# Kernel tuning notes

Measured on AMD Instinct MI355X. Metric: run time of the kernel, lower is better.

The kernel has to match this reference:

```python
import jax, jax.numpy as jnp
import numpy as np
import math

B, S, E, H, F, L, V = 4, 256, 512, 8, 2048, 4, 32000
HD = E // H
MAXLEN = 5000  # EnhancedPositionalEncoding max_len default


def _ln(x, s, b):
    m = jnp.mean(x, axis=-1, keepdims=True)
    v = jnp.mean((x - m) ** 2, axis=-1, keepdims=True)
    return (x - m) / jnp.sqrt(v + 1e-5) * s + b


def setup_inputs() -> dict:
    key = jax.random.key(0)
    ks = jax.random.split(key, 10)
    n = lambda k, shape: jax.random.normal(k, shape, jnp.float32) * 0.02
    return {
        "src": jax.random.randint(ks[0], (B, S), 0, V),
        "emb": jax.random.uniform(ks[1], (V, E), jnp.float32, -0.1, 0.1),
        "rel_table": n(ks[2], (2 * MAXLEN - 1, E)),
        "norm_in_s": jnp.ones(E, jnp.float32), "norm_in_b": jnp.zeros(E, jnp.float32),
        "inW": n(ks[3], (L, 3 * E, E)), "inB": jnp.zeros((L, 3 * E), jnp.float32),
        "outW": n(ks[4], (L, E, E)), "outB": jnp.zeros((L, E), jnp.float32),
        "ln1_s": jnp.ones((L, E), jnp.float32), "ln1_b": jnp.zeros((L, E), jnp.float32),
        "ln2_s": jnp.ones((L, E), jnp.float32), "ln2_b": jnp.zeros((L, E), jnp.float32),
        "w1": n(ks[5], (L, F, E)), "b1": jnp.zeros((L, F), jnp.float32),
        "w2": n(ks[6], (L, E, F)), "b2": jnp.zeros((L, E), jnp.float32),
        "normf_s": jnp.ones(E, jnp.float32), "normf_b": jnp.zeros(E, jnp.float32),
        "dec_w": jax.random.uniform(ks[7], (V, E), jnp.float32, -0.1, 0.1),
        "dec_b": jnp.zeros(V, jnp.float32),
    }


def reference(src, emb, rel_table, norm_in_s, norm_in_b, inW, inB, outW, outB,
              ln1_s, ln1_b, ln2_s, ln2_b, w1, b1, w2, b2, normf_s, normf_b,
              dec_w, dec_b):
    x = emb[src] * math.sqrt(E)                 # [B,S,E], pos_encoder is identity in relative mode
    x = _ln(x, norm_in_s, norm_in_b)
    # relative-position embedding gather: idx[l,m] = (m - l) + S - 1
    pos = jnp.arange(S)
    rel_idx = (pos[None, :] - pos[:, None]) + S - 1
    rel = rel_table[rel_idx].reshape(S, S, H, HD)  # [S,S,H,hd]
    # NOTE: torch adds the BOOL triu mask to float scores -> +1.0 at masked positions
    mask = jnp.triu(jnp.ones((S, S), jnp.float32), 1)
    scale = 1.0 / math.sqrt(HD)
    for l in range(L):
        h = _ln(x, ln1_s[l], ln1_b[l])
        qkv = h @ inW[l].T + inB[l]
        q, k, v = jnp.split(qkv, 3, axis=-1)
        q = q.reshape(B, S, H, HD).transpose(0, 2, 1, 3)  # [B,H,S,hd]
        k = k.reshape(B, S, H, HD).transpose(0, 2, 1, 3)
        v = v.reshape(B, S, H, HD).transpose(0, 2, 1, 3)
        scores = jnp.einsum('bhqd,bhkd->bhqk', q, k) * scale
        bias = jnp.einsum('bhld,lmhd->bhlm', q, rel)      # relative-position bias (unscaled, as in torch)
        attn = jax.nn.softmax(scores + bias + mask, axis=-1)
        o = jnp.einsum('bhqk,bhkd->bhqd', attn, v).transpose(0, 2, 1, 3).reshape(B, S, E)
        x = x + (o @ outW[l].T + outB[l])
        h2 = _ln(x, ln2_s[l], ln2_b[l])
        ff = jax.nn.gelu(h2 @ w1[l].T + b1[l], approximate=False) @ w2[l].T + b2[l]
        x = x + ff
    x = _ln(x, normf_s, normf_b)  # encoder final norm
    return x @ dec_w.T + dec_b    # [B,S,V]
```

## Files before the change

kernel.cpp:

```cpp
#include <hip/hip_runtime.h>
#include <hip/hip_bf16.h>
#include <math.h>

#define BB 4
#define SS 256
#define EE 512
#define HH 8
#define HD 64
#define FFD 2048
#define LL 4
#define VV 32000
#define BS (BB*SS)
#define SQRT_E 22.627416997969522f
#define ATTN_SCALE 0.125f

typedef __bf16 bf16;
typedef __attribute__((ext_vector_type(4))) __bf16 bf16x4;
typedef __attribute__((ext_vector_type(8))) __bf16 bf16x8;
typedef __attribute__((ext_vector_type(4))) float f32x4;

#define GLOBAL_AS __attribute__((address_space(1)))
#define LDS_AS    __attribute__((address_space(3)))

__device__ __forceinline__ void load_lds16(const bf16* g, bf16* l) {
    __builtin_amdgcn_global_load_lds((const GLOBAL_AS unsigned int*)g,
                                     (LDS_AS unsigned int*)l, 16, 0, 0);
}

__global__ void cvt_bf16(const float* __restrict__ in, bf16* __restrict__ out, int n) {
    int i = (blockIdx.x * 256 + threadIdx.x) * 4;
    if (i < n) {
        float4 v = *(const float4*)(in + i);
        bf16x4 o;
        o[0] = (bf16)v.x; o[1] = (bf16)v.y; o[2] = (bf16)v.z; o[3] = (bf16)v.w;
        *(bf16x4*)(out + i) = o;
    }
}

template <typename OT>
__global__ void ln_kernel(const float* __restrict__ in, const float* __restrict__ sc,
                          const float* __restrict__ bi, OT* __restrict__ out) {
    int row = blockIdx.x;
    int t = threadIdx.x;
    const float* r = in + (size_t)row * EE;
    float v0 = r[t], v1 = r[t + 256];
    float sum = v0 + v1, sq = v0 * v0 + v1 * v1;
    #pragma unroll
    for (int off = 32; off; off >>= 1) {
        sum += __shfl_xor(sum, off);
        sq  += __shfl_xor(sq, off);
    }
    __shared__ float ssum[4], ssq[4];
    int wid = t >> 6, lane = t & 63;
    if (lane == 0) { ssum[wid] = sum; ssq[wid] = sq; }
    __syncthreads();
    sum = ssum[0] + ssum[1] + ssum[2] + ssum[3];
    sq  = ssq[0] + ssq[1] + ssq[2] + ssq[3];
    float mean = sum * (1.0f / EE);
    float var  = sq * (1.0f / EE) - mean * mean;
    float rstd = rsqrtf(var + 1e-5f);
    out[(size_t)row * EE + t]       = (OT)((v0 - mean) * rstd * sc[t] + bi[t]);
    out[(size_t)row * EE + t + 256] = (OT)((v1 - mean) * rstd * sc[t + 256] + bi[t + 256]);
}

__global__ void embed_ln_kernel(const int* __restrict__ src, const float* __restrict__ emb,
                                const float* __restrict__ sc, const float* __restrict__ bi,
                                float* __restrict__ out) {
    int row = blockIdx.x;
    int t = threadIdx.x;
    const float* r = emb + (size_t)src[row] * EE;
    float v0 = r[t] * SQRT_E, v1 = r[t + 256] * SQRT_E;
    float sum = v0 + v1, sq = v0 * v0 + v1 * v1;
    #pragma unroll
    for (int off = 32; off; off >>= 1) {
        sum += __shfl_xor(sum, off);
        sq  += __shfl_xor(sq, off);
    }
    __shared__ float ssum[4], ssq[4];
    int wid = t >> 6, lane = t & 63;
    if (lane == 0) { ssum[wid] = sum; ssq[wid] = sq; }
    __syncthreads();
    sum = ssum[0] + ssum[1] + ssum[2] + ssum[3];
    sq  = ssq[0] + ssq[1] + ssq[2] + ssq[3];
    float mean = sum * (1.0f / EE);
    float var  = sq * (1.0f / EE) - mean * mean;
    float rstd = rsqrtf(var + 1e-5f);
    out[(size_t)row * EE + t]       = (v0 - mean) * rstd * sc[t] + bi[t];
    out[(size_t)row * EE + t + 256] = (v1 - mean) * rstd * sc[t + 256] + bi[t + 256];
}

template <int BM, int BN, int MODE, int OBF16>
__global__ __launch_bounds__(256) void gemm_bf16(
        const bf16* __restrict__ A, const bf16* __restrict__ W,
        const float* __restrict__ bias, void* __restrict__ Cout,
        const float* __restrict__ res, int M, int N, int K) {
    constexpr int FM = BM / 32, FN = BN / 32;
    __shared__ bf16 Atile[BM * 32];
    __shared__ bf16 Btile[BN * 32];
    int tid = threadIdx.x;
    int wid = tid >> 6, lane = tid & 63;
    int wm = (wid >> 1) * (BM / 2), wn = (wid & 1) * (BN / 2);
    int bm = blockIdx.x * BM, bn = blockIdx.y * BN;

    f32x4 acc[FM][FN];
    #pragma unroll
    for (int i = 0; i < FM; i++)
        #pragma unroll
        for (int j = 0; j < FN; j++)
            acc[i][j] = (f32x4){0.f, 0.f, 0.f, 0.f};

    int mrow = lane & 15, kq = (lane >> 4) * 8;

    for (int k0 = 0; k0 < K; k0 += 32) {
        #pragma unroll
        for (int it = 0; it < BM / 64; it++) {
            int c = it * 256 + tid;
            int row = c >> 2, kc = (c & 3) * 8;
            load_lds16(A + (size_t)(bm + row) * K + k0 + kc, Atile + c * 8);
        }
        #pragma unroll
        for (int it = 0; it < BN / 64; it++) {
            int c = it * 256 + tid;
            int row = c >> 2, kc = (c & 3) * 8;
            load_lds16(W + (size_t)(bn + row) * K + k0 + kc, Btile + c * 8);
        }
        __syncthreads();

        bf16x8 af[FM], bfv[FN];
        #pragma unroll
        for (int i = 0; i < FM; i++)
            af[i] = *(const bf16x8*)(Atile + (wm + i * 16 + mrow) * 32 + kq);
        #pragma unroll
        for (int j = 0; j < FN; j++)
            bfv[j] = *(const bf16x8*)(Btile + (wn + j * 16 + mrow) * 32 + kq);
        #pragma unroll
        for (int i = 0; i < FM; i++)
            #pragma unroll
            for (int j = 0; j < FN; j++)
                acc[i][j] = __builtin_amdgcn_mfma_f32_16x16x32_bf16(af[i], bfv[j], acc[i][j], 0, 0, 0);
        __syncthreads();
    }

    #pragma unroll
    for (int i = 0; i < FM; i++) {
        int row0 = bm + wm + i * 16 + (lane >> 4) * 4;
        #pragma unroll
        for (int j = 0; j < FN; j++) {
            int col = bn + wn + j * 16 + (lane & 15);
            float bv = bias[col];
            #pragma unroll
            for (int r = 0; r < 4; r++) {
                int row = row0 + r;
                float v = acc[i][j][r] + bv;
                if (MODE == 1) v = 0.5f * v * (1.0f + erff(v * 0.7071067811865476f));
                if (MODE == 2) v += res[(size_t)row * N + col];
                if (OBF16) ((bf16*)Cout)[(size_t)row * N + col] = (bf16)v;
                else       ((float*)Cout)[(size_t)row * N + col] = v;
            }
        }
    }
}

__global__ __launch_bounds__(256) void transpose_v(const bf16* __restrict__ qkv,
                                                   bf16* __restrict__ vT) {
    int bh = blockIdx.x, kc = blockIdx.y;
    int b = bh >> 3, h = bh & 7;
    __shared__ __align__(16) bf16 tile[64 * 72];
    int t = threadIdx.x;
    #pragma unroll
    for (int it = 0; it < 2; it++) {
        int c = it * 256 + t; int r = c >> 3, ch = c & 7;
        bf16x8 v = *(const bf16x8*)(qkv + (size_t)(b * 256 + kc * 64 + r) * 1536 + 1024 + h * 64 + ch * 8);
        *(bf16x8*)(tile + r * 72 + ch * 8) = v;
    }
    __syncthreads();
    #pragma unroll
    for (int it = 0; it < 2; it++) {
        int c = it * 256 + t; int n = c >> 3, kch = c & 7;
        bf16x8 o;
        #pragma unroll
        for (int j = 0; j < 8; j++) o[j] = tile[(kch * 8 + j) * 72 + n];
        *(bf16x8*)(vT + ((size_t)(bh * 64 + n)) * 256 + kc * 64 + kch * 8) = o;
    }
}

__global__ __launch_bounds__(256) void attn_mfma(const bf16* __restrict__ qkv,
        const bf16* __restrict__ relb, const bf16* __restrict__ vT,
        bf16* __restrict__ o) {
    int blk = blockIdx.x;
    int qt = blk & 3, bh = blk >> 2;
    int h = bh & 7, b = bh >> 3;
    int q0 = qt * 64, j0 = 192 - q0;
    int tid = threadIdx.x;
    int wid = tid >> 6, lane = tid & 63;
    int l15 = lane & 15, quad = lane >> 4;
    int mr0 = wid * 16;

    __shared__ __align__(16) bf16 Qs[64 * 72];
    __shared__ __align__(16) bf16 Stg[64 * 72];
    __shared__ __align__(16) bf16 BP[64 * 264];

    const size_t qbase = (size_t)(b * 256 + q0) * 1536 + h * 64;
    #pragma unroll
    for (int it = 0; it < 2; it++) {
        int c = it * 256 + tid; int r = c >> 3, ch = c & 7;
        bf16x8 v = *(const bf16x8*)(qkv + qbase + (size_t)r * 1536 + ch * 8);
        *(bf16x8*)(Qs + r * 72 + ch * 8) = v;
    }
    __syncthreads();
    bf16x8 af0 = *(const bf16x8*)(Qs + (mr0 + l15) * 72 + quad * 8);
    bf16x8 af1 = *(const bf16x8*)(Qs + (mr0 + l15) * 72 + 32 + quad * 8);

    for (int jc = 0; jc < 5; jc++) {
        __syncthreads();
        const size_t rbase = (size_t)(j0 + jc * 64) * 512 + h * 64;
        #pragma unroll
        for (int it = 0; it < 2; it++) {
            int c = it * 256 + tid; int r = c >> 3, ch = c & 7;
            bf16x8 v = *(const bf16x8*)(relb + rbase + (size_t)r * 512 + ch * 8);
            *(bf16x8*)(Stg + r * 72 + ch * 8) = v;
        }
        __syncthreads();
        #pragma unroll
        for (int jt = 0; jt < 4; jt++) {
            f32x4 acc = (f32x4){0.f, 0.f, 0.f, 0.f};
            bf16x8 bv0 = *(const bf16x8*)(Stg + (jt * 16 + l15) * 72 + quad * 8);
            bf16x8 bv1 = *(const bf16x8*)(Stg + (jt * 16 + l15) * 72 + 32 + quad * 8);
            acc = __builtin_amdgcn_mfma_f32_16x16x32_bf16(af0, bv0, acc, 0, 0, 0);
            acc = __builtin_amdgcn_mfma_f32_16x16x32_bf16(af1, bv1, acc, 0, 0, 0);
            int jp = jc * 64 + jt * 16 + l15;
            #pragma unroll
            for (int r = 0; r < 4; r++) {
                int ll = mr0 + quad * 4 + r;
                int m = jp + ll - 63;
                if (m >= 0 && m < 256) BP[ll * 256 + m] = (bf16)acc[r];
            }
        }
    }

    f32x4 S[16];
    #pragma unroll
    for (int i = 0; i < 16; i++) S[i] = (f32x4){0.f, 0.f, 0.f, 0.f};
    for (int kc = 0; kc < 4; kc++) {
        __syncthreads();
        const size_t kbase = (size_t)(b * 256 + kc * 64) * 1536 + 512 + h * 64;
        #pragma unroll
        for (int it = 0; it < 2; it++) {
            int c = it * 256 + tid; int r = c >> 3, ch = c & 7;
            bf16x8 v = *(const bf16x8*)(qkv + kbase + (size_t)r * 1536 + ch * 8);
            *(bf16x8*)(Stg + r * 72 + ch * 8) = v;
        }
        __syncthreads();
        #pragma unroll
        for (int nt = 0; nt < 4; nt++) {
            bf16x8 bv0 = *(const bf16x8*)(Stg + (nt * 16 + l15) * 72 + quad * 8);
            bf16x8 bv1 = *(const bf16x8*)(Stg + (nt * 16 + l15) * 72 + 32 + quad * 8);
            S[kc * 4 + nt] = __builtin_amdgcn_mfma_f32_16x16x32_bf16(af0, bv0, S[kc * 4 + nt], 0, 0, 0);
            S[kc * 4 + nt] = __builtin_amdgcn_mfma_f32_16x16x32_bf16(af1, bv1, S[kc * 4 + nt], 0, 0, 0);
        }
    }

    float rmax[4] = {-1e30f, -1e30f, -1e30f, -1e30f};
    #pragma unroll
    for (int T = 0; T < 16; T++) {
        int m = T * 16 + l15;
        #pragma unroll
        for (int r = 0; r < 4; r++) {
            int ll = mr0 + quad * 4 + r;
            float v = S[T][r] * ATTN_SCALE + (float)BP[ll * 256 + m]
                      + ((m > q0 + ll) ? 1.0f : 0.0f);
            S[T][r] = v;
            rmax[r] = fmaxf(rmax[r], v);
        }
    }
    #pragma unroll
    for (int r = 0; r < 4; r++)
        #pragma unroll
        for (int d = 1; d < 16; d <<= 1)
            rmax[r] = fmaxf(rmax[r], __shfl_xor(rmax[r], d));
    float rsum[4] = {0.f, 0.f, 0.f, 0.f};
    #pragma unroll
    for (int T = 0; T < 16; T++)
        #pragma unroll
        for (int r = 0; r < 4; r++) {
            float p = expf(S[T][r] - rmax[r]);
            S[T][r] = p;
            rsum[r] += p;
        }
    #pragma unroll
    for (int r = 0; r < 4; r++)
        #pragma unroll
        for (int d = 1; d < 16; d <<= 1)
            rsum[r] += __shfl_xor(rsum[r], d);

    __syncthreads();
    #pragma unroll
    for (int T = 0; T < 16; T++)
        #pragma unroll
        for (int r = 0; r < 4; r++)
            BP[(mr0 + quad * 4 + r) * 264 + T * 16 + l15] = (bf16)S[T][r];

    f32x4 oacc[4];
    #pragma unroll
    for (int i = 0; i < 4; i++) oacc[i] = (f32x4){0.f, 0.f, 0.f, 0.f};
    for (int kc = 0; kc < 4; kc++) {
        __syncthreads();
        const size_t vb = (size_t)(bh * 64) * 256 + kc * 64;
        #pragma unroll
        for (int it = 0; it < 2; it++) {
            int c = it * 256 + tid; int r = c >> 3, ch = c & 7;
            bf16x8 v = *(const bf16x8*)(vT + vb + (size_t)r * 256 + ch * 8);
            *(bf16x8*)(Stg + r * 72 + ch * 8) = v;
        }
        __syncthreads();
        #pragma unroll
        for (int ks = 0; ks < 2; ks++) {
            bf16x8 ap = *(const bf16x8*)(BP + (mr0 + l15) * 264 + kc * 64 + ks * 32 + quad * 8);
            #pragma unroll
            for (int nt = 0; nt < 4; nt++) {
                bf16x8 bv = *(const bf16x8*)(Stg + (nt * 16 + l15) * 72 + ks * 32 + quad * 8);
                oacc[nt] = __builtin_amdgcn_mfma_f32_16x16x32_bf16(ap, bv, oacc[nt], 0, 0, 0);
            }
        }
    }

    #pragma unroll
    for (int nt = 0; nt < 4; nt++)
        #pragma unroll
        for (int r = 0; r < 4; r++) {
            int ll = mr0 + quad * 4 + r;
            o[(size_t)(b * 256 + q0 + ll) * 512 + h * 64 + nt * 16 + l15] =
                (bf16)(oacc[nt][r] * (1.0f / rsum[r]));
        }
}

template <int MODE>
__global__ void gemm_nt(const float* __restrict__ A, const float* __restrict__ W,
                        const float* __restrict__ bias, float* __restrict__ C,
                        const float* __restrict__ res, int M, int N, int K) {
    __shared__ float As[64][17];
    __shared__ float Ws[64][17];
    int tid = threadIdx.x;
    int tx = tid & 15, ty = tid >> 4;
    int bm = blockIdx.y * 64, bn = blockIdx.x * 64;
    float acc[4][4] = {};
    for (int k0 = 0; k0 < K; k0 += 16) {
        #pragma unroll
        for (int i = 0; i < 4; i++) {
            int idx = tid + i * 256;
            int r = idx >> 4, c = idx & 15;
            As[r][c] = A[(size_t)(bm + r) * K + k0 + c];
            Ws[r][c] = W[(size_t)(bn + r) * K + k0 + c];
        }
        __syncthreads();
        #pragma unroll
        for (int kk = 0; kk < 16; kk++) {
            float a[4], w[4];
            #pragma unroll
            for (int i = 0; i < 4; i++) a[i] = As[ty * 4 + i][kk];
            #pragma unroll
            for (int j = 0; j < 4; j++) w[j] = Ws[tx * 4 + j][kk];
            #pragma unroll
            for (int i = 0; i < 4; i++)
                #pragma unroll
                for (int j = 0; j < 4; j++)
                    acc[i][j] += a[i] * w[j];
        }
        __syncthreads();
    }
    #pragma unroll
    for (int i = 0; i < 4; i++) {
        int row = bm + ty * 4 + i;
        #pragma unroll
        for (int j = 0; j < 4; j++) {
            int col = bn + tx * 4 + j;
            float v = acc[i][j] + bias[col];
            if (MODE == 1) v = 0.5f * v * (1.0f + erff(v * 0.7071067811865476f));
            if (MODE == 2) v += res[(size_t)row * N + col];
            C[(size_t)row * N + col] = v;
        }
    }
}

__global__ void attn_kernel(const float* __restrict__ qkv, const float* __restrict__ rel_table,
                            float* __restrict__ o) {
    int blk = blockIdx.x;
    int l = blk & (SS - 1);
    int bh = blk >> 8;
    int h = bh & (HH - 1);
    int b = bh >> 3;
    int t = threadIdx.x;
    int wid = t >> 6, lane = t & 63;

    __shared__ float qs[HD];
    __shared__ float attn_s[SS];
    __shared__ float swave[4];
    __shared__ float opart[4][HD];

    const float* qrow = qkv + (size_t)(b * SS + l) * (3 * EE) + h * HD;
    if (t < HD) qs[t] = qrow[t];
    __syncthreads();

    const float* krow   = qkv + (size_t)(b * SS + t) * (3 * EE) + EE + h * HD;
    const float* relrow = rel_table + (size_t)(t - l + SS - 1) * EE + h * HD;
    const float4* k4 = reinterpret_cast<const float4*>(krow);
    const float4* r4 = reinterpret_cast<const float4*>(relrow);
    float s1 = 0.f, s2 = 0.f;
    #pragma unroll
    for (int d4 = 0; d4 < HD / 4; d4++) {
        float4 kv = k4[d4], rv = r4[d4];
        float q0 = qs[4 * d4], q1 = qs[4 * d4 + 1], q2 = qs[4 * d4 + 2], q3 = qs[4 * d4 + 3];
        s1 += q0 * kv.x + q1 * kv.y + q2 * kv.z + q3 * kv.w;
        s2 += q0 * rv.x + q1 * rv.y + q2 * rv.z + q3 * rv.w;
    }
    float val = s1 * ATTN_SCALE + s2 + ((t > l) ? 1.0f : 0.0f);

    float m = val;
    #pragma unroll
    for (int off = 32; off; off >>= 1) m = fmaxf(m, __shfl_xor(m, off));
    if (lane == 0) swave[wid] = m;
    __syncthreads();
    m = fmaxf(fmaxf(swave[0], swave[1]), fmaxf(swave[2], swave[3]));
    float p = expf(val - m);
    float s = p;
    #pragma unroll
    for (int off = 32; off; off >>= 1) s += __shfl_xor(s, off);
    __syncthreads();
    if (lane == 0) swave[wid] = s;
    __syncthreads();
    float tot = swave[0] + swave[1] + swave[2] + swave[3];
    attn_s[t] = p;
    __syncthreads();

    int d = t & 63, part = t >> 6;
    const float* vbase = qkv + (size_t)(b * SS) * (3 * EE) + 2 * EE + h * HD + d;
    float acc = 0.f;
    int m0 = part * 64;
    #pragma unroll 8
    for (int mm = m0; mm < m0 + 64; mm++)
        acc += attn_s[mm] * vbase[(size_t)mm * (3 * EE)];
    opart[part][d] = acc;
    __syncthreads();
    if (t < 64) {
        float ov = (opart[0][d] + opart[1][d] + opart[2][d] + opart[3][d]) / tot;
        o[(size_t)(b * SS + l) * EE + h * HD + d] = ov;
    }
}

extern "C" void kernel_launch(void* const* d_in, const int* in_sizes, int n_in,
                              void* d_out, int out_size, void* d_ws, size_t ws_size,
                              hipStream_t stream) {
    const int*   src    = (const int*)  d_in[0];
    const float* emb    = (const float*)d_in[1];
    const float* rel    = (const float*)d_in[2];
    const float* nin_s  = (const float*)d_in[3];
    const float* nin_b  = (const float*)d_in[4];
    const float* inW    = (const float*)d_in[5];
    const float* inB    = (const float*)d_in[6];
    const float* outW   = (const float*)d_in[7];
    const float* outB   = (const float*)d_in[8];
    const float* ln1_s  = (const float*)d_in[9];
    const float* ln1_b  = (const float*)d_in[10];
    const float* ln2_s  = (const float*)d_in[11];
    const float* ln2_b  = (const float*)d_in[12];
    const float* w1     = (const float*)d_in[13];
    const float* b1     = (const float*)d_in[14];
    const float* w2     = (const float*)d_in[15];
    const float* b2     = (const float*)d_in[16];
    const float* normf_s= (const float*)d_in[17];
    const float* normf_b= (const float*)d_in[18];
    const float* dec_w  = (const float*)d_in[19];
    const float* dec_b  = (const float*)d_in[20];
    float* out = (float*)d_out;

    const size_t n_inW  = (size_t)LL * 3 * EE * EE;
    const size_t n_outW = (size_t)LL * EE * EE;
    const size_t n_w1   = (size_t)LL * FFD * EE;
    const size_t n_w2   = (size_t)LL * EE * FFD;
    const size_t n_dec  = (size_t)VV * EE;
    const size_t n_rel  = (size_t)511 * EE;

    float* x    = (float*)d_ws;
    bf16*  qkvb = (bf16*)(x + (size_t)BS * EE);
    bf16*  hb   = qkvb + (size_t)BS * 3 * EE;
    bf16*  ob   = hb + (size_t)BS * EE;
    bf16*  ffb  = ob + (size_t)BS * EE;
    bf16*  vTb  = ffb + (size_t)BS * FFD;
    bf16*  relb = vTb + (size_t)BS * 512;
    bf16*  inWb  = relb + (size_t)512 * EE;
    bf16*  outWb = inWb + n_inW;
    bf16*  w1b   = outWb + n_outW;
    bf16*  w2b   = w1b + n_w1;
    bf16*  decWb = w2b + n_w2;
    size_t needed = (size_t)((char*)(decWb + n_dec) - (char*)d_ws);

    if (ws_size >= needed) {
        cvt_bf16<<<(int)(n_inW  / 1024), 256, 0, stream>>>(inW,   inWb,  (int)n_inW);
        cvt_bf16<<<(int)(n_outW / 1024), 256, 0, stream>>>(outW,  outWb, (int)n_outW);
        cvt_bf16<<<(int)(n_w1   / 1024), 256, 0, stream>>>(w1,    w1b,   (int)n_w1);
        cvt_bf16<<<(int)(n_w2   / 1024), 256, 0, stream>>>(w2,    w2b,   (int)n_w2);
        cvt_bf16<<<(int)(n_dec  / 1024), 256, 0, stream>>>(dec_w, decWb, (int)n_dec);
        cvt_bf16<<<(int)((n_rel + 1023) / 1024), 256, 0, stream>>>(rel, relb, (int)n_rel);

        embed_ln_kernel<<<BS, 256, 0, stream>>>(src, emb, nin_s, nin_b, x);

        for (int l = 0; l < LL; l++) {
            ln_kernel<bf16><<<BS, 256, 0, stream>>>(x, ln1_s + l * EE, ln1_b + l * EE, hb);
            gemm_bf16<64, 64, 0, 1><<<dim3(BS / 64, 3 * EE / 64), 256, 0, stream>>>(
                hb, inWb + (size_t)l * 3 * EE * EE, inB + (size_t)l * 3 * EE, qkvb, nullptr,
                BS, 3 * EE, EE);
            transpose_v<<<dim3(BB * HH, 4), 256, 0, stream>>>(qkvb, vTb);
            attn_mfma<<<BB * HH * 4, 256, 0, stream>>>(qkvb, relb, vTb, ob);
            gemm_bf16<64, 64, 2, 0><<<dim3(BS / 64, EE / 64), 256, 0, stream>>>(
                ob, outWb + (size_t)l * EE * EE, outB + (size_t)l * EE, x, x,
                BS, EE, EE);
            ln_kernel<bf16><<<BS, 256, 0, stream>>>(x, ln2_s + l * EE, ln2_b + l * EE, hb);
            gemm_bf16<64, 64, 1, 1><<<dim3(BS / 64, FFD / 64), 256, 0, stream>>>(
                hb, w1b + (size_t)l * FFD * EE, b1 + (size_t)l * FFD, ffb, nullptr,
                BS, FFD, EE);
            gemm_bf16<64, 64, 2, 0><<<dim3(BS / 64, EE / 64), 256, 0, stream>>>(
                ffb, w2b + (size_t)l * EE * FFD, b2 + (size_t)l * EE, x, x,
                BS, EE, FFD);
        }

        ln_kernel<bf16><<<BS, 256, 0, stream>>>(x, normf_s, normf_b, hb);
        gemm_bf16<128, 128, 0, 0><<<dim3(BS / 128, VV / 128), 256, 0, stream>>>(
            hb, decWb, dec_b, out, nullptr, BS, VV, EE);
    } else {
        float* h     = x + (size_t)BS * EE;
        float* qkvf  = h + (size_t)BS * EE;
        float* o     = qkvf + (size_t)BS * 3 * EE;
        float* ffmid = o + (size_t)BS * EE;

        embed_ln_kernel<<<BS, 256, 0, stream>>>(src, emb, nin_s, nin_b, x);
        for (int l = 0; l < LL; l++) {
            ln_kernel<float><<<BS, 256, 0, stream>>>(x, ln1_s + l * EE, ln1_b + l * EE, h);
            gemm_nt<0><<<dim3(3 * EE / 64, BS / 64), 256, 0, stream>>>(
                h, inW + (size_t)l * 3 * EE * EE, inB + (size_t)l * 3 * EE, qkvf, nullptr,
                BS, 3 * EE, EE);
            attn_kernel<<<BB * HH * SS, 256, 0, stream>>>(qkvf, rel, o);
            gemm_nt<2><<<dim3(EE / 64, BS / 64), 256, 0, stream>>>(
                o, outW + (size_t)l * EE * EE, outB + (size_t)l * EE, x, x,
                BS, EE, EE);
            ln_kernel<float><<<BS, 256, 0, stream>>>(x, ln2_s + l * EE, ln2_b + l * EE, h);
            gemm_nt<1><<<dim3(FFD / 64, BS / 64), 256, 0, stream>>>(
                h, w1 + (size_t)l * FFD * EE, b1 + (size_t)l * FFD, ffmid, nullptr,
                BS, FFD, EE);
            gemm_nt<2><<<dim3(EE / 64, BS / 64), 256, 0, stream>>>(
                ffmid, w2 + (size_t)l * EE * FFD, b2 + (size_t)l * EE, x, x,
                BS, EE, FFD);
        }
        ln_kernel<float><<<BS, 256, 0, stream>>>(x, normf_s, normf_b, h);
        gemm_nt<0><<<dim3(VV / 64, BS / 64), 256, 0, stream>>>(
            h, dec_w, dec_b, out, nullptr, BS, VV, EE);
    }
}
```

Before: 673.5 us.

## Double-buffer GEMM tiles, fuse V transpose and weight converts, prefetch attention tiles

Several changes land together. The six weight-conversion launches merge into one kernel, and the V transpose moves into the QKV GEMM epilogue so that kernel goes away. The GEMM gets a double-buffered LDS pipeline, and the decoder GEMM gets an XCD-aware block swizzle. The attention kernel prefetches its next rel/K/V tile into registers while computing the current one. The aim is fewer launches and latency hidden behind MFMA work, at the cost of twice the LDS and strided scattered stores for vT.

```diff
diff --git a/kernel.cpp b/kernel.cpp
--- a/kernel.cpp
+++ b/kernel.cpp
@@ -27,13 +27,26 @@
                                      (LDS_AS unsigned int*)l, 16, 0, 0);
 }
 
-__global__ void cvt_bf16(const float* __restrict__ in, bf16* __restrict__ out, int n) {
-    int i = (blockIdx.x * 256 + threadIdx.x) * 4;
+__global__ void cvt_all(const float* __restrict__ inW, const float* __restrict__ outW,
+                        const float* __restrict__ w1, const float* __restrict__ w2,
+                        const float* __restrict__ dec, const float* __restrict__ rel,
+                        bf16* __restrict__ inWb, bf16* __restrict__ outWb,
+                        bf16* __restrict__ w1b, bf16* __restrict__ w2b,
+                        bf16* __restrict__ decb, bf16* __restrict__ relb) {
+    int b = blockIdx.x;
+    const float* s; bf16* d; int base; int n;
+    if (b < 3072)       { s = inW;  d = inWb;  base = b;         n = 3145728; }
+    else if (b < 4096)  { s = outW; d = outWb; base = b - 3072;  n = 1048576; }
+    else if (b < 8192)  { s = w1;   d = w1b;   base = b - 4096;  n = 4194304; }
+    else if (b < 12288) { s = w2;   d = w2b;   base = b - 8192;  n = 4194304; }
+    else if (b < 28288) { s = dec;  d = decb;  base = b - 12288; n = 16384000; }
+    else                { s = rel;  d = relb;  base = b - 28288; n = 261632; }
+    int i = (base * 256 + threadIdx.x) * 4;
     if (i < n) {
-        float4 v = *(const float4*)(in + i);
+        float4 v = *(const float4*)(s + i);
         bf16x4 o;
         o[0] = (bf16)v.x; o[1] = (bf16)v.y; o[2] = (bf16)v.z; o[3] = (bf16)v.w;
-        *(bf16x4*)(out + i) = o;
+        *(bf16x4*)(d + i) = o;
     }
 }
 
@@ -89,18 +102,32 @@
     out[(size_t)row * EE + t + 256] = (v1 - mean) * rstd * sc[t + 256] + bi[t + 256];
 }
 
-template <int BM, int BN, int MODE, int OBF16>
+template <int BM, int BN, int MODE, int OBF16, int WRVT, int SWZ>
 __global__ __launch_bounds__(256) void gemm_bf16(
         const bf16* __restrict__ A, const bf16* __restrict__ W,
         const float* __restrict__ bias, void* __restrict__ Cout,
-        const float* __restrict__ res, int M, int N, int K) {
+        const float* __restrict__ res, bf16* __restrict__ vT,
+        int M, int N, int K) {
     constexpr int FM = BM / 32, FN = BN / 32;
-    __shared__ bf16 Atile[BM * 32];
-    __shared__ bf16 Btile[BN * 32];
+    __shared__ bf16 Atile[2][BM * 32];
+    __shared__ bf16 Btile[2][BN * 32];
     int tid = threadIdx.x;
     int wid = tid >> 6, lane = tid & 63;
     int wm = (wid >> 1) * (BM / 2), wn = (wid & 1) * (BN / 2);
-    int bm = blockIdx.x * BM, bn = blockIdx.y * BN;
+    int bm, bn;
+    if (SWZ) {
+        int nbm = gridDim.x;
+        int linear = blockIdx.y * nbm + blockIdx.x;
+        int total = nbm * gridDim.y;
+        int chunk = total >> 3;
+        int xcd = linear & 7, idx = linear >> 3;
+        int g = xcd * chunk + idx;
+        bm = (g % nbm) * BM;
+        bn = (g / nbm) * BN;
+    } else {
+        bm = blockIdx.x * BM;
+        bn = blockIdx.y * BN;
+    }
 
     f32x4 acc[FM][FN];
     #pragma unroll
@@ -111,34 +138,40 @@
 
     int mrow = lane & 15, kq = (lane >> 4) * 8;
 
-    for (int k0 = 0; k0 < K; k0 += 32) {
+    auto stage = [&](int buf, int k0) {
         #pragma unroll
         for (int it = 0; it < BM / 64; it++) {
             int c = it * 256 + tid;
             int row = c >> 2, kc = (c & 3) * 8;
-            load_lds16(A + (size_t)(bm + row) * K + k0 + kc, Atile + c * 8);
+            load_lds16(A + (size_t)(bm + row) * K + k0 + kc, &Atile[buf][c * 8]);
         }
         #pragma unroll
         for (int it = 0; it < BN / 64; it++) {
             int c = it * 256 + tid;
             int row = c >> 2, kc = (c & 3) * 8;
-            load_lds16(W + (size_t)(bn + row) * K + k0 + kc, Btile + c * 8);
-        }
-        __syncthreads();
-
+            load_lds16(W + (size_t)(bn + row) * K + k0 + kc, &Btile[buf][c * 8]);
+        }
+    };
+
+    stage(0, 0);
+    __syncthreads();
+    int cur = 0;
+    for (int k0 = 0; k0 < K; k0 += 32) {
+        if (k0 + 32 < K) stage(cur ^ 1, k0 + 32);
         bf16x8 af[FM], bfv[FN];
         #pragma unroll
         for (int i = 0; i < FM; i++)
-            af[i] = *(const bf16x8*)(Atile + (wm + i * 16 + mrow) * 32 + kq);
+            af[i] = *(const bf16x8*)(&Atile[cur][(wm + i * 16 + mrow) * 32 + kq]);
         #pragma unroll
         for (int j = 0; j < FN; j++)
-            bfv[j] = *(const bf16x8*)(Btile + (wn + j * 16 + mrow) * 32 + kq);
+            bfv[j] = *(const bf16x8*)(&Btile[cur][(wn + j * 16 + mrow) * 32 + kq]);
         #pragma unroll
         for (int i = 0; i < FM; i++)
             #pragma unroll
             for (int j = 0; j < FN; j++)
                 acc[i][j] = __builtin_amdgcn_mfma_f32_16x16x32_bf16(af[i], bfv[j], acc[i][j], 0, 0, 0);
         __syncthreads();
+        cur ^= 1;
     }
 
     #pragma unroll
@@ -154,33 +187,13 @@
                 float v = acc[i][j][r] + bv;
                 if (MODE == 1) v = 0.5f * v * (1.0f + erff(v * 0.7071067811865476f));
                 if (MODE == 2) v += res[(size_t)row * N + col];
-                if (OBF16) ((bf16*)Cout)[(size_t)row * N + col] = (bf16)v;
-                else       ((float*)Cout)[(size_t)row * N + col] = v;
+                if (WRVT && col >= 1024) {
+                    int cc = col - 1024;
+                    vT[(size_t)(((row >> 8) * 8 + (cc >> 6)) * 64 + (cc & 63)) * 256 + (row & 255)] = (bf16)v;
+                } else if (OBF16) ((bf16*)Cout)[(size_t)row * N + col] = (bf16)v;
+                else              ((float*)Cout)[(size_t)row * N + col] = v;
             }
         }
-    }
-}
-
-__global__ __launch_bounds__(256) void transpose_v(const bf16* __restrict__ qkv,
-                                                   bf16* __restrict__ vT) {
-    int bh = blockIdx.x, kc = blockIdx.y;
-    int b = bh >> 3, h = bh & 7;
-    __shared__ __align__(16) bf16 tile[64 * 72];
-    int t = threadIdx.x;
-    #pragma unroll
-    for (int it = 0; it < 2; it++) {
-        int c = it * 256 + t; int r = c >> 3, ch = c & 7;
-        bf16x8 v = *(const bf16x8*)(qkv + (size_t)(b * 256 + kc * 64 + r) * 1536 + 1024 + h * 64 + ch * 8);
-        *(bf16x8*)(tile + r * 72 + ch * 8) = v;
-    }
-    __syncthreads();
-    #pragma unroll
-    for (int it = 0; it < 2; it++) {
-        int c = it * 256 + t; int n = c >> 3, kch = c & 7;
-        bf16x8 o;
-        #pragma unroll
-        for (int j = 0; j < 8; j++) o[j] = tile[(kch * 8 + j) * 72 + n];
-        *(bf16x8*)(vT + ((size_t)(bh * 64 + n)) * 256 + kc * 64 + kch * 8) = o;
     }
 }
 
@@ -200,27 +213,42 @@
     __shared__ __align__(16) bf16 Stg[64 * 72];
     __shared__ __align__(16) bf16 BP[64 * 264];
 
+    int c0 = tid, c1 = 256 + tid;
+    int r0 = c0 >> 3, ch0 = (c0 & 7) * 8;
+    int r1 = c1 >> 3, ch1 = (c1 & 7) * 8;
+
     const size_t qbase = (size_t)(b * 256 + q0) * 1536 + h * 64;
-    #pragma unroll
-    for (int it = 0; it < 2; it++) {
-        int c = it * 256 + tid; int r = c >> 3, ch = c & 7;
-        bf16x8 v = *(const bf16x8*)(qkv + qbase + (size_t)r * 1536 + ch * 8);
-        *(bf16x8*)(Qs + r * 72 + ch * 8) = v;
-    }
+    *(bf16x8*)(Qs + r0 * 72 + ch0) = *(const bf16x8*)(qkv + qbase + (size_t)r0 * 1536 + ch0);
+    *(bf16x8*)(Qs + r1 * 72 + ch1) = *(const bf16x8*)(qkv + qbase + (size_t)r1 * 1536 + ch1);
+
+    bf16x8 pf0, pf1;
+    {
+        const size_t rb = (size_t)j0 * 512 + h * 64;
+        pf0 = *(const bf16x8*)(relb + rb + (size_t)r0 * 512 + ch0);
+        pf1 = *(const bf16x8*)(relb + rb + (size_t)r1 * 512 + ch1);
+    }
+
     __syncthreads();
     bf16x8 af0 = *(const bf16x8*)(Qs + (mr0 + l15) * 72 + quad * 8);
     bf16x8 af1 = *(const bf16x8*)(Qs + (mr0 + l15) * 72 + 32 + quad * 8);
 
+    f32x4 S[16];
+    #pragma unroll
+    for (int i = 0; i < 16; i++) S[i] = (f32x4){0.f, 0.f, 0.f, 0.f};
+
     for (int jc = 0; jc < 5; jc++) {
-        __syncthreads();
-        const size_t rbase = (size_t)(j0 + jc * 64) * 512 + h * 64;
-        #pragma unroll
-        for (int it = 0; it < 2; it++) {
-            int c = it * 256 + tid; int r = c >> 3, ch = c & 7;
-            bf16x8 v = *(const bf16x8*)(relb + rbase + (size_t)r * 512 + ch * 8);
-            *(bf16x8*)(Stg + r * 72 + ch * 8) = v;
-        }
-        __syncthreads();
+        *(bf16x8*)(Stg + r0 * 72 + ch0) = pf0;
+        *(bf16x8*)(Stg + r1 * 72 + ch1) = pf1;
+        __syncthreads();
+        if (jc < 4) {
+            const size_t rb = (size_t)(j0 + (jc + 1) * 64) * 512 + h * 64;
+            pf0 = *(const bf16x8*)(relb + rb + (size_t)r0 * 512 + ch0);
+            pf1 = *(const bf16x8*)(relb + rb + (size_t)r1 * 512 + ch1);
+        } else {
+            const size_t kb = (size_t)(b * 256) * 1536 + 512 + h * 64;
+            pf0 = *(const bf16x8*)(qkv + kb + (size_t)r0 * 1536 + ch0);
+            pf1 = *(const bf16x8*)(qkv + kb + (size_t)r1 * 1536 + ch1);
+        }
         #pragma unroll
         for (int jt = 0; jt < 4; jt++) {
             f32x4 acc = (f32x4){0.f, 0.f, 0.f, 0.f};
@@ -236,21 +264,22 @@
                 if (m >= 0 && m < 256) BP[ll * 256 + m] = (bf16)acc[r];
             }
         }
-    }
-
-    f32x4 S[16];
-    #pragma unroll
-    for (int i = 0; i < 16; i++) S[i] = (f32x4){0.f, 0.f, 0.f, 0.f};
+        __syncthreads();
+    }
+
     for (int kc = 0; kc < 4; kc++) {
-        __syncthreads();
-        const size_t kbase = (size_t)(b * 256 + kc * 64) * 1536 + 512 + h * 64;
-        #pragma unroll
-        for (int it = 0; it < 2; it++) {
-            int c = it * 256 + tid; int r = c >> 3, ch = c & 7;
-            bf16x8 v = *(const bf16x8*)(qkv + kbase + (size_t)r * 1536 + ch * 8);
-            *(bf16x8*)(Stg + r * 72 + ch * 8) = v;
-        }
-        __syncthreads();
+        *(bf16x8*)(Stg + r0 * 72 + ch0) = pf0;
+        *(bf16x8*)(Stg + r1 * 72 + ch1) = pf1;
+        __syncthreads();
+        if (kc < 3) {
+            const size_t kb = (size_t)(b * 256 + (kc + 1) * 64) * 1536 + 512 + h * 64;
+            pf0 = *(const bf16x8*)(qkv + kb + (size_t)r0 * 1536 + ch0);
+            pf1 = *(const bf16x8*)(qkv + kb + (size_t)r1 * 1536 + ch1);
+        } else {
+            const size_t vb = (size_t)(bh * 64) * 256;
+            pf0 = *(const bf16x8*)(vT + vb + (size_t)r0 * 256 + ch0);
+            pf1 = *(const bf16x8*)(vT + vb + (size_t)r1 * 256 + ch1);
+        }
         #pragma unroll
         for (int nt = 0; nt < 4; nt++) {
             bf16x8 bv0 = *(const bf16x8*)(Stg + (nt * 16 + l15) * 72 + quad * 8);
@@ -258,6 +287,7 @@
             S[kc * 4 + nt] = __builtin_amdgcn_mfma_f32_16x16x32_bf16(af0, bv0, S[kc * 4 + nt], 0, 0, 0);
             S[kc * 4 + nt] = __builtin_amdgcn_mfma_f32_16x16x32_bf16(af1, bv1, S[kc * 4 + nt], 0, 0, 0);
         }
+        __syncthreads();
     }
 
     float rmax[4] = {-1e30f, -1e30f, -1e30f, -1e30f};
@@ -304,15 +334,14 @@
     #pragma unroll
     for (int i = 0; i < 4; i++) oacc[i] = (f32x4){0.f, 0.f, 0.f, 0.f};
     for (int kc = 0; kc < 4; kc++) {
-        __syncthreads();
-        const size_t vb = (size_t)(bh * 64) * 256 + kc * 64;
-        #pragma unroll
-        for (int it = 0; it < 2; it++) {
-            int c = it * 256 + tid; int r = c >> 3, ch = c & 7;
-            bf16x8 v = *(const bf16x8*)(vT + vb + (size_t)r * 256 + ch * 8);
-            *(bf16x8*)(Stg + r * 72 + ch * 8) = v;
-        }
-        __syncthreads();
+        *(bf16x8*)(Stg + r0 * 72 + ch0) = pf0;
+        *(bf16x8*)(Stg + r1 * 72 + ch1) = pf1;
+        __syncthreads();
+        if (kc < 3) {
+            const size_t vb = (size_t)(bh * 64) * 256 + (kc + 1) * 64;
+            pf0 = *(const bf16x8*)(vT + vb + (size_t)r0 * 256 + ch0);
+            pf1 = *(const bf16x8*)(vT + vb + (size_t)r1 * 256 + ch1);
+        }
         #pragma unroll
         for (int ks = 0; ks < 2; ks++) {
             bf16x8 ap = *(const bf16x8*)(BP + (mr0 + l15) * 264 + kc * 64 + ks * 32 + quad * 8);
@@ -322,6 +351,7 @@
                 oacc[nt] = __builtin_amdgcn_mfma_f32_16x16x32_bf16(ap, bv, oacc[nt], 0, 0, 0);
             }
         }
+        __syncthreads();
     }
 
     #pragma unroll
@@ -478,7 +508,6 @@
     const size_t n_w1   = (size_t)LL * FFD * EE;
     const size_t n_w2   = (size_t)LL * EE * FFD;
     const size_t n_dec  = (size_t)VV * EE;
-    const size_t n_rel  = (size_t)511 * EE;
 
     float* x    = (float*)d_ws;
     bf16*  qkvb = (bf16*)(x + (size_t)BS * EE);
@@ -495,37 +524,31 @@
     size_t needed = (size_t)((char*)(decWb + n_dec) - (char*)d_ws);
 
     if (ws_size >= needed) {
-        cvt_bf16<<<(int)(n_inW  / 1024), 256, 0, stream>>>(inW,   inWb,  (int)n_inW);
-        cvt_bf16<<<(int)(n_outW / 1024), 256, 0, stream>>>(outW,  outWb, (int)n_outW);
-        cvt_bf16<<<(int)(n_w1   / 1024), 256, 0, stream>>>(w1,    w1b,   (int)n_w1);
-        cvt_bf16<<<(int)(n_w2   / 1024), 256, 0, stream>>>(w2,    w2b,   (int)n_w2);
-        cvt_bf16<<<(int)(n_dec  / 1024), 256, 0, stream>>>(dec_w, decWb, (int)n_dec);
-        cvt_bf16<<<(int)((n_rel + 1023) / 1024), 256, 0, stream>>>(rel, relb, (int)n_rel);
-
         embed_ln_kernel<<<BS, 256, 0, stream>>>(src, emb, nin_s, nin_b, x);
+        cvt_all<<<28544, 256, 0, stream>>>(inW, outW, w1, w2, dec_w, rel,
+                                           inWb, outWb, w1b, w2b, decWb, relb);
 
         for (int l = 0; l < LL; l++) {
             ln_kernel<bf16><<<BS, 256, 0, stream>>>(x, ln1_s + l * EE, ln1_b + l * EE, hb);
-            gemm_bf16<64, 64, 0, 1><<<dim3(BS / 64, 3 * EE / 64), 256, 0, stream>>>(
+            gemm_bf16<64, 64, 0, 1, 1, 0><<<dim3(BS / 64, 3 * EE / 64), 256, 0, stream>>>(
                 hb, inWb + (size_t)l * 3 * EE * EE, inB + (size_t)l * 3 * EE, qkvb, nullptr,
-                BS, 3 * EE, EE);
-            transpose_v<<<dim3(BB * HH, 4), 256, 0, stream>>>(qkvb, vTb);
+                vTb, BS, 3 * EE, EE);
             attn_mfma<<<BB * HH * 4, 256, 0, stream>>>(qkvb, relb, vTb, ob);
-            gemm_bf16<64, 64, 2, 0><<<dim3(BS / 64, EE / 64), 256, 0, stream>>>(
+            gemm_bf16<64, 64, 2, 0, 0, 0><<<dim3(BS / 64, EE / 64), 256, 0, stream>>>(
                 ob, outWb + (size_t)l * EE * EE, outB + (size_t)l * EE, x, x,
-                BS, EE, EE);
+                nullptr, BS, EE, EE);
             ln_kernel<bf16><<<BS, 256, 0, stream>>>(x, ln2_s + l * EE, ln2_b + l * EE, hb);
-            gemm_bf16<64, 64, 1, 1><<<dim3(BS / 64, FFD / 64), 256, 0, stream>>>(
+            gemm_bf16<64, 64, 1, 1, 0, 0><<<dim3(BS / 64, FFD / 64), 256, 0, stream>>>(
                 hb, w1b + (size_t)l * FFD * EE, b1 + (size_t)l * FFD, ffb, nullptr,
-                BS, FFD, EE);
-            gemm_bf16<64, 64, 2, 0><<<dim3(BS / 64, EE / 64), 256, 0, stream>>>(
+                nullptr, BS, FFD, EE);
+            gemm_bf16<64, 64, 2, 0, 0, 0><<<dim3(BS / 64, EE / 64), 256, 0, stream>>>(
                 ffb, w2b + (size_t)l * EE * FFD, b2 + (size_t)l * EE, x, x,
-                BS, EE, FFD);
+                nullptr, BS, EE, FFD);
         }
 
         ln_kernel<bf16><<<BS, 256, 0, stream>>>(x, normf_s, normf_b, hb);
-        gemm_bf16<128, 128, 0, 0><<<dim3(BS / 128, VV / 128), 256, 0, stream>>>(
-            hb, decWb, dec_b, out, nullptr, BS, VV, EE);
+        gemm_bf16<128, 128, 0, 0, 0, 1><<<dim3(BS / 128, VV / 128), 256, 0, stream>>>(
+            hb, decWb, dec_b, out, nullptr, nullptr, BS, VV, EE);
     } else {
         float* h     = x + (size_t)BS * EE;
         float* qkvf  = h + (size_t)BS * EE;
```

Result: faster. 621.7 us (-7.7%).
